# Kernel tuning notes

Hardware: AMD Instinct MI355X
Metric: run time of the kernel (lower is better)

The kernel has to match this reference:

```python
import jax, jax.numpy as jnp
import numpy as np

ITERATIONS = 25  # skeleton_iterations
EPS = 1e-6


def _dilate(x):
    # 3x3 max-pool, stride 1, SAME padding (pads with -inf, matching torch max_pool2d)
    return jax.lax.reduce_window(x, -jnp.inf, jax.lax.max,
                                 (1, 1, 3, 3), (1, 1, 1, 1), 'SAME')


def _erode(x):
    return -_dilate(-x)


def _soft_skeleton(img):
    # img: (B,1,H,W) probability map
    img = jnp.clip(img, 0.0, 1.0)
    skel = jax.nn.relu(img - _dilate(_erode(img)))

    def body(_, carry):
        im, sk = carry
        im = _erode(im)
        delta = jax.nn.relu(im - _dilate(_erode(im)))
        sk = sk + jax.nn.relu(delta - sk * delta)
        return (im, sk)

    _, skel = jax.lax.fori_loop(0, ITERATIONS - 1, body, (img, skel))
    return skel


def setup_inputs() -> dict:
    key = jax.random.key(0)
    k1, k2 = jax.random.split(key)
    B, C, H, W = 8, 19, 512, 512
    return {
        'student_logits': jax.random.normal(k1, (B, C, H, W), dtype=jnp.float32),
        'sam3_pseudo_mask': jax.random.uniform(k2, (B, H, W), dtype=jnp.float32),
        'class_index': 1,
    }


def reference(student_logits, sam3_pseudo_mask, class_index):
    # student probability for target class: (B,1,H,W)
    student_prob = jax.nn.softmax(student_logits, axis=1)[:, class_index:class_index + 1]
    teacher_prob = jnp.clip(sam3_pseudo_mask[:, None, :, :], 0.0, 1.0)

    student_skel = _soft_skeleton(student_prob)
    teacher_skel = _soft_skeleton(teacher_prob)

    rd = (1, 2, 3)
    tprec = (jnp.sum(student_skel * teacher_prob, axis=rd) + EPS) / (jnp.sum(student_skel, axis=rd) + EPS)
    tsens = (jnp.sum(teacher_skel * student_prob, axis=rd) + EPS) / (jnp.sum(teacher_skel, axis=rd) + EPS)
    cldice = (2.0 * tprec * tsens + EPS) / (tprec + tsens + EPS)
    return jnp.mean(1.0 - cldice)
```

## Files before the change

kernel.cpp:

```cpp
#include <hip/hip_runtime.h>

#define B 8
#define C 19
#define H 512
#define W 512
#define P (H*W)
#define NPL 16
#define BIGF 1e30f
#define NT 512
#define HR 14
#define SR 92
#define SC 96
#define E  13

__device__ __forceinline__ float min3f(float a, float b, float c) { return fminf(fminf(a, b), c); }
__device__ __forceinline__ float max3f(float a, float b, float c) { return fmaxf(fmaxf(a, b), c); }

__global__ __launch_bounds__(256) void prep_kernel(
    const float* __restrict__ logits, const float* __restrict__ mask,
    const int* __restrict__ cls, float* __restrict__ prob)
{
    int tid = blockIdx.x * 256 + threadIdx.x;
    const int tot = B * (P / 4);
    if (tid >= tot) return;
    int b  = tid / (P / 4);
    int i4 = tid % (P / 4);
    int ci = *cls;

    const float4* lg = reinterpret_cast<const float4*>(logits) + (size_t)b * C * (P / 4) + i4;
    float4 v[C];
    float4 vc = make_float4(0.f, 0.f, 0.f, 0.f);
    #pragma unroll
    for (int c = 0; c < C; ++c) {
        float4 t = lg[(size_t)c * (P / 4)];
        v[c] = t;
        if (c == ci) vc = t;
    }
    float4 mx = v[0];
    #pragma unroll
    for (int c = 1; c < C; ++c) {
        mx.x = fmaxf(mx.x, v[c].x); mx.y = fmaxf(mx.y, v[c].y);
        mx.z = fmaxf(mx.z, v[c].z); mx.w = fmaxf(mx.w, v[c].w);
    }
    float4 s = make_float4(0.f, 0.f, 0.f, 0.f);
    #pragma unroll
    for (int c = 0; c < C; ++c) {
        s.x += expf(v[c].x - mx.x); s.y += expf(v[c].y - mx.y);
        s.z += expf(v[c].z - mx.z); s.w += expf(v[c].w - mx.w);
    }
    float4 p;
    p.x = expf(vc.x - mx.x) / s.x;
    p.y = expf(vc.y - mx.y) / s.y;
    p.z = expf(vc.z - mx.z) / s.z;
    p.w = expf(vc.w - mx.w) / s.w;

    float4* pr = reinterpret_cast<float4*>(prob);
    pr[(size_t)b * (P / 4) + i4] = p;

    float4 tm = reinterpret_cast<const float4*>(mask)[(size_t)b * (P / 4) + i4];
    tm.x = fminf(fmaxf(tm.x, 0.f), 1.f);
    tm.y = fminf(fmaxf(tm.y, 0.f), 1.f);
    tm.z = fminf(fmaxf(tm.z, 0.f), 1.f);
    tm.w = fminf(fmaxf(tm.w, 0.f), 1.f);
    pr[(size_t)(8 + b) * (P / 4) + i4] = tm;
}

__device__ __forceinline__ void erode_pass(const float* __restrict__ src,
                                           float* __restrict__ dst, int p, int tid)
{
    const int r0 = p;
    const int n  = (SR - 2 * p) * 24;
    const int lane = tid & 63;
    for (int idx = tid; idx < n; idx += NT) {
        int r = r0 + idx / 24, g = idx % 24, c = 4 * g;
        const float* s1 = src + r * SC + c;
        float4 a  = *reinterpret_cast<const float4*>(s1 - SC);
        float4 b  = *reinterpret_cast<const float4*>(s1);
        float4 cc = *reinterpret_cast<const float4*>(s1 + SC);
        float4 vm;
        vm.x = min3f(a.x, b.x, cc.x);
        vm.y = min3f(a.y, b.y, cc.y);
        vm.z = min3f(a.z, b.z, cc.z);
        vm.w = min3f(a.w, b.w, cc.w);
        float vL = __shfl_up(vm.w, 1);
        float vR = __shfl_down(vm.x, 1);
        if (g == 0  || lane == 0)  vL = min3f(s1[-SC - 1], s1[-1], s1[SC - 1]);
        if (g == 23 || lane == 63) vR = min3f(s1[-SC + 4], s1[4], s1[SC + 4]);
        float4 o;
        o.x = min3f(vL,   vm.x, vm.y);
        o.y = min3f(vm.x, vm.y, vm.z);
        o.z = min3f(vm.y, vm.z, vm.w);
        o.w = min3f(vm.z, vm.w, vR);
        *reinterpret_cast<float4*>(dst + r * SC + c) = o;
    }
}

__device__ __forceinline__ float4 dilate4(const float* __restrict__ e,
                                          int lr, int lc, int gy, int gxb,
                                          bool fbL, bool fbR)
{
    const float* p0 = e + (lr - 1) * SC + lc;
    const float* p1 = e + lr * SC + lc;
    const float* p2 = e + (lr + 1) * SC + lc;
    float4 a = *reinterpret_cast<const float4*>(p0);
    float4 b = *reinterpret_cast<const float4*>(p1);
    float4 c = *reinterpret_cast<const float4*>(p2);
    const bool t = (gy > 0), u = (gy < H - 1);
    float4 vm;
    vm.x = fmaxf(b.x, fmaxf(t ? a.x : -BIGF, u ? c.x : -BIGF));
    vm.y = fmaxf(b.y, fmaxf(t ? a.y : -BIGF, u ? c.y : -BIGF));
    vm.z = fmaxf(b.z, fmaxf(t ? a.z : -BIGF, u ? c.z : -BIGF));
    vm.w = fmaxf(b.w, fmaxf(t ? a.w : -BIGF, u ? c.w : -BIGF));
    float vL = __shfl_up(vm.w, 1);
    float vR = __shfl_down(vm.x, 1);
    if (fbL) vL = max3f(t ? p0[-1] : -BIGF, p1[-1], u ? p2[-1] : -BIGF);
    if (fbR) vR = max3f(t ? p0[4]  : -BIGF, p1[4],  u ? p2[4]  : -BIGF);
    if (gxb == 0)     vL = -BIGF;
    if (gxb == W - 4) vR = -BIGF;
    float4 d;
    d.x = max3f(vL,   vm.x, vm.y);
    d.y = max3f(vm.x, vm.y, vm.z);
    d.z = max3f(vm.y, vm.z, vm.w);
    d.w = max3f(vm.z, vm.w, vR);
    return d;
}

template<int MODE>
__global__ __launch_bounds__(NT, 4) void skel_kernel(
    const float* __restrict__ in, float* __restrict__ im_out,
    float* __restrict__ gsk, const float* __restrict__ prob,
    double* __restrict__ sums)
{
    __shared__ __align__(16) float lds[2 * SR * SC + 32];
    float* const bx = lds + 16;
    float* const by = bx + SR * SC;
    const int pl  = blockIdx.z;
    const int ty0 = blockIdx.y * 64, tx0 = blockIdx.x * 64;
    const int tid = threadIdx.x;
    const float* ip = in + (size_t)pl * P;
    const size_t gbase = (size_t)pl * P;

    const int jA  = tid & 15;
    const int pyA = tid >> 4, pyB = pyA + 32;
    const int lcA = 16 + 4 * jA;
    const int lrA = pyA + HR, lrB = pyB + HR;
    const int gyA = ty0 + pyA, gyB = ty0 + pyB;
    const int gxb = tx0 + 4 * jA;
    const bool fbL = (jA == 0)  || ((tid & 63) == 0);
    const bool fbR = (jA == 15) || ((tid & 63) == 63);

    const bool xin = (tx0 >= 16) && (tx0 <= W - 80);
    for (int idx = tid; idx < SR * 24; idx += NT) {
        int r = idx / 24, g = idx % 24;
        int gy = ty0 - HR + r; gy = min(max(gy, 0), H - 1);
        int gx0 = tx0 - 16 + 4 * g;
        float4 v;
        if (xin) {
            v = *reinterpret_cast<const float4*>(ip + (size_t)gy * W + gx0);
        } else {
            const float* rp = ip + (size_t)gy * W;
            v.x = rp[min(max(gx0,     0), W - 1)];
            v.y = rp[min(max(gx0 + 1, 0), W - 1)];
            v.z = rp[min(max(gx0 + 2, 0), W - 1)];
            v.w = rp[min(max(gx0 + 3, 0), W - 1)];
        }
        *reinterpret_cast<float4*>(&bx[r * SC + 4 * g]) = v;
    }

    float4 sk0, sk1;
    if (MODE == 0) {
        sk0 = make_float4(0.f, 0.f, 0.f, 0.f);
        sk1 = sk0;
    } else {
        sk0 = *reinterpret_cast<const float4*>(gsk + gbase + (size_t)gyA * W + gxb);
        sk1 = *reinterpret_cast<const float4*>(gsk + gbase + (size_t)gyB * W + gxb);
    }
    __syncthreads();

    erode_pass(bx, by, 1, tid);
    float4 curA = *reinterpret_cast<const float4*>(bx + lrA * SC + lcA);
    float4 curB = *reinterpret_cast<const float4*>(bx + lrB * SC + lcA);
    __syncthreads();

    for (int p = 2; p <= E; ++p) {
        const float* src = (p & 1) ? bx : by;
        float*       dst = (p & 1) ? by : bx;
        if (MODE == 0 || p > 2) {
            float4 dA = dilate4(src, lrA, lcA, gyA, gxb, fbL, fbR);
            float4 dB = dilate4(src, lrB, lcA, gyB, gxb, fbL, fbR);
            float4 del;
            del.x = fmaxf(curA.x - dA.x, 0.f); del.y = fmaxf(curA.y - dA.y, 0.f);
            del.z = fmaxf(curA.z - dA.z, 0.f); del.w = fmaxf(curA.w - dA.w, 0.f);
            sk0.x += fmaxf(del.x - sk0.x * del.x, 0.f);
            sk0.y += fmaxf(del.y - sk0.y * del.y, 0.f);
            sk0.z += fmaxf(del.z - sk0.z * del.z, 0.f);
            sk0.w += fmaxf(del.w - sk0.w * del.w, 0.f);
            del.x = fmaxf(curB.x - dB.x, 0.f); del.y = fmaxf(curB.y - dB.y, 0.f);
            del.z = fmaxf(curB.z - dB.z, 0.f); del.w = fmaxf(curB.w - dB.w, 0.f);
            sk1.x += fmaxf(del.x - sk1.x * del.x, 0.f);
            sk1.y += fmaxf(del.y - sk1.y * del.y, 0.f);
            sk1.z += fmaxf(del.z - sk1.z * del.z, 0.f);
            sk1.w += fmaxf(del.w - sk1.w * del.w, 0.f);
        }
        float4 nxtA = *reinterpret_cast<const float4*>(src + lrA * SC + lcA);
        float4 nxtB = *reinterpret_cast<const float4*>(src + lrB * SC + lcA);
        erode_pass(src, dst, p, tid);
        __syncthreads();
        curA = nxtA; curB = nxtB;
    }

    {
        float4 dA = dilate4(by, lrA, lcA, gyA, gxb, fbL, fbR);
        float4 dB = dilate4(by, lrB, lcA, gyB, gxb, fbL, fbR);
        float4 del;
        del.x = fmaxf(curA.x - dA.x, 0.f); del.y = fmaxf(curA.y - dA.y, 0.f);
        del.z = fmaxf(curA.z - dA.z, 0.f); del.w = fmaxf(curA.w - dA.w, 0.f);
        sk0.x += fmaxf(del.x - sk0.x * del.x, 0.f);
        sk0.y += fmaxf(del.y - sk0.y * del.y, 0.f);
        sk0.z += fmaxf(del.z - sk0.z * del.z, 0.f);
        sk0.w += fmaxf(del.w - sk0.w * del.w, 0.f);
        del.x = fmaxf(curB.x - dB.x, 0.f); del.y = fmaxf(curB.y - dB.y, 0.f);
        del.z = fmaxf(curB.z - dB.z, 0.f); del.w = fmaxf(curB.w - dB.w, 0.f);
        sk1.x += fmaxf(del.x - sk1.x * del.x, 0.f);
        sk1.y += fmaxf(del.y - sk1.y * del.y, 0.f);
        sk1.z += fmaxf(del.z - sk1.z * del.z, 0.f);
        sk1.w += fmaxf(del.w - sk1.w * del.w, 0.f);
    }

    if (MODE == 0) {
        *reinterpret_cast<float4*>(im_out + gbase + (size_t)gyA * W + gxb) = curA;
        *reinterpret_cast<float4*>(im_out + gbase + (size_t)gyB * W + gxb) = curB;
        *reinterpret_cast<float4*>(gsk + gbase + (size_t)gyA * W + gxb) = sk0;
        *reinterpret_cast<float4*>(gsk + gbase + (size_t)gyB * W + gxb) = sk1;
    } else {
        const float* op = prob + (size_t)(pl ^ 8) * P;
        float4 tA = *reinterpret_cast<const float4*>(op + (size_t)gyA * W + gxb);
        float4 tB = *reinterpret_cast<const float4*>(op + (size_t)gyB * W + gxb);
        float a0 = sk0.x * tA.x + sk0.y * tA.y + sk0.z * tA.z + sk0.w * tA.w
                 + sk1.x * tB.x + sk1.y * tB.y + sk1.z * tB.z + sk1.w * tB.w;
        float a1 = sk0.x + sk0.y + sk0.z + sk0.w + sk1.x + sk1.y + sk1.z + sk1.w;
        #pragma unroll
        for (int off = 32; off > 0; off >>= 1) {
            a0 += __shfl_down(a0, off);
            a1 += __shfl_down(a1, off);
        }
        __syncthreads();
        float* scratch = lds;
        int wv = tid >> 6, ln = tid & 63;
        if (ln == 0) { scratch[wv * 2] = a0; scratch[wv * 2 + 1] = a1; }
        __syncthreads();
        if (tid == 0) {
            double s0 = 0.0, s1 = 0.0;
            for (int w = 0; w < NT / 64; ++w) {
                s0 += (double)scratch[w * 2];
                s1 += (double)scratch[w * 2 + 1];
            }
            int b = pl & 7, base = (pl < 8) ? 0 : 2;
            atomicAdd(&sums[b * 4 + base + 0], s0);
            atomicAdd(&sums[b * 4 + base + 1], s1);
        }
    }
}

__global__ void zero_sums_kernel(double* __restrict__ sums)
{
    if (threadIdx.x < 32) sums[threadIdx.x] = 0.0;
}

__global__ void final_kernel(const double* __restrict__ sums, float* __restrict__ out)
{
    if (threadIdx.x == 0) {
        double acc = 0.0;
        for (int b = 0; b < 8; ++b) {
            double tprec = (sums[b * 4 + 0] + 1e-6) / (sums[b * 4 + 1] + 1e-6);
            double tsens = (sums[b * 4 + 2] + 1e-6) / (sums[b * 4 + 3] + 1e-6);
            double cl    = (2.0 * tprec * tsens + 1e-6) / (tprec + tsens + 1e-6);
            acc += 1.0 - cl;
        }
        out[0] = (float)(acc / 8.0);
    }
}

extern "C" void kernel_launch(void* const* d_in, const int* in_sizes, int n_in,
                              void* d_out, int out_size, void* d_ws, size_t ws_size,
                              hipStream_t stream)
{
    const float* logits = (const float*)d_in[0];
    const float* mask   = (const float*)d_in[1];
    const int*   cls    = (const int*)d_in[2];
    float* out = (float*)d_out;

    float*  ws   = (float*)d_ws;
    float*  prob = ws;
    float*  imA  = ws + (size_t)16 * P;
    float*  gsk  = ws + (size_t)32 * P;
    double* sums = (double*)(ws + (size_t)48 * P);

    dim3 sg(8, 8, NPL);
    zero_sums_kernel<<<1, 64, 0, stream>>>(sums);
    prep_kernel<<<(B * (P / 4) + 255) / 256, 256, 0, stream>>>(logits, mask, cls, prob);
    skel_kernel<0><<<sg, NT, 0, stream>>>(prob, imA, gsk, prob, sums);
    skel_kernel<2><<<sg, NT, 0, stream>>>(imA, nullptr, gsk, prob, sums);
    final_kernel<<<1, 64, 0, stream>>>(sums, out);
}
```

Measured before the change: 384.0 us.

## Fuse dilate with erode per thread-owned pixels and split halo erode work

Inside the skeleton loop, each thread now computes the erode of its two owned 4-pixel groups and, from the same three LDS row loads, the dilate used for the skeleton update. This removes the separate dilate pass's LDS re-reads and the extra center load. Remaining halo columns and rows are eroded by a separate mapping: the extra column groups plus a shrinking set of top and bottom halo rows. Zeroing of the sums buffer moves into the prep kernel, dropping one launch. The new work split changes load balance across threads and adds index logic.

```diff
diff --git a/kernel.cpp b/kernel.cpp
--- a/kernel.cpp
+++ b/kernel.cpp
@@ -15,11 +15,14 @@
 
 __device__ __forceinline__ float min3f(float a, float b, float c) { return fminf(fminf(a, b), c); }
 __device__ __forceinline__ float max3f(float a, float b, float c) { return fmaxf(fmaxf(a, b), c); }
+__device__ __forceinline__ float4 ld4(const float* p) { return *reinterpret_cast<const float4*>(p); }
 
 __global__ __launch_bounds__(256) void prep_kernel(
     const float* __restrict__ logits, const float* __restrict__ mask,
-    const int* __restrict__ cls, float* __restrict__ prob)
-{
+    const int* __restrict__ cls, float* __restrict__ prob,
+    double* __restrict__ sums)
+{
+    if (blockIdx.x == 0 && threadIdx.x < 32) sums[threadIdx.x] = 0.0;
     int tid = blockIdx.x * 256 + threadIdx.x;
     const int tot = B * (P / 4);
     if (tid >= tot) return;
@@ -65,64 +68,110 @@
     pr[(size_t)(8 + b) * (P / 4) + i4] = tm;
 }
 
-__device__ __forceinline__ void erode_pass(const float* __restrict__ src,
-                                           float* __restrict__ dst, int p, int tid)
-{
-    const int r0 = p;
-    const int n  = (SR - 2 * p) * 24;
-    const int lane = tid & 63;
-    for (int idx = tid; idx < n; idx += NT) {
-        int r = r0 + idx / 24, g = idx % 24, c = 4 * g;
-        const float* s1 = src + r * SC + c;
-        float4 a  = *reinterpret_cast<const float4*>(s1 - SC);
-        float4 b  = *reinterpret_cast<const float4*>(s1);
-        float4 cc = *reinterpret_cast<const float4*>(s1 + SC);
-        float4 vm;
-        vm.x = min3f(a.x, b.x, cc.x);
-        vm.y = min3f(a.y, b.y, cc.y);
-        vm.z = min3f(a.z, b.z, cc.z);
-        vm.w = min3f(a.w, b.w, cc.w);
-        float vL = __shfl_up(vm.w, 1);
-        float vR = __shfl_down(vm.x, 1);
-        if (g == 0  || lane == 0)  vL = min3f(s1[-SC - 1], s1[-1], s1[SC - 1]);
-        if (g == 23 || lane == 63) vR = min3f(s1[-SC + 4], s1[4], s1[SC + 4]);
-        float4 o;
-        o.x = min3f(vL,   vm.x, vm.y);
-        o.y = min3f(vm.x, vm.y, vm.z);
-        o.z = min3f(vm.y, vm.z, vm.w);
-        o.w = min3f(vm.z, vm.w, vR);
-        *reinterpret_cast<float4*>(dst + r * SC + c) = o;
-    }
-}
-
-__device__ __forceinline__ float4 dilate4(const float* __restrict__ e,
-                                          int lr, int lc, int gy, int gxb,
-                                          bool fbL, bool fbR)
-{
-    const float* p0 = e + (lr - 1) * SC + lc;
-    const float* p1 = e + lr * SC + lc;
-    const float* p2 = e + (lr + 1) * SC + lc;
-    float4 a = *reinterpret_cast<const float4*>(p0);
-    float4 b = *reinterpret_cast<const float4*>(p1);
-    float4 c = *reinterpret_cast<const float4*>(p2);
-    const bool t = (gy > 0), u = (gy < H - 1);
+__device__ __forceinline__ float4 erode_grp(const float* __restrict__ src,
+                                            int r, int c, bool fL, bool fR)
+{
+    const float* s1 = src + r * SC + c;
+    float4 a = ld4(s1 - SC), b = ld4(s1), cc = ld4(s1 + SC);
     float4 vm;
-    vm.x = fmaxf(b.x, fmaxf(t ? a.x : -BIGF, u ? c.x : -BIGF));
-    vm.y = fmaxf(b.y, fmaxf(t ? a.y : -BIGF, u ? c.y : -BIGF));
-    vm.z = fmaxf(b.z, fmaxf(t ? a.z : -BIGF, u ? c.z : -BIGF));
-    vm.w = fmaxf(b.w, fmaxf(t ? a.w : -BIGF, u ? c.w : -BIGF));
+    vm.x = min3f(a.x, b.x, cc.x);
+    vm.y = min3f(a.y, b.y, cc.y);
+    vm.z = min3f(a.z, b.z, cc.z);
+    vm.w = min3f(a.w, b.w, cc.w);
     float vL = __shfl_up(vm.w, 1);
     float vR = __shfl_down(vm.x, 1);
-    if (fbL) vL = max3f(t ? p0[-1] : -BIGF, p1[-1], u ? p2[-1] : -BIGF);
-    if (fbR) vR = max3f(t ? p0[4]  : -BIGF, p1[4],  u ? p2[4]  : -BIGF);
-    if (gxb == 0)     vL = -BIGF;
-    if (gxb == W - 4) vR = -BIGF;
+    if (fL) vL = min3f(s1[-SC - 1], s1[-1], s1[SC - 1]);
+    if (fR) vR = min3f(s1[-SC + 4], s1[4], s1[SC + 4]);
+    float4 o;
+    o.x = min3f(vL,   vm.x, vm.y);
+    o.y = min3f(vm.x, vm.y, vm.z);
+    o.z = min3f(vm.y, vm.z, vm.w);
+    o.w = min3f(vm.z, vm.w, vR);
+    return o;
+}
+
+template<bool DODIL>
+__device__ __forceinline__ float4 fused_grp(const float* __restrict__ src,
+    int lr, int c, int gy, int gxb, bool fL, bool fR,
+    float4* __restrict__ bcap, float4* __restrict__ dil)
+{
+    const float* s1 = src + lr * SC + c;
+    float4 a = ld4(s1 - SC), b = ld4(s1), cc = ld4(s1 + SC);
+    *bcap = b;
+    float eL0 = 0.f, eL1 = 0.f, eL2 = 0.f, eR0 = 0.f, eR1 = 0.f, eR2 = 0.f;
+    if (fL) { eL0 = s1[-SC - 1]; eL1 = s1[-1]; eL2 = s1[SC - 1]; }
+    if (fR) { eR0 = s1[-SC + 4]; eR1 = s1[4];  eR2 = s1[SC + 4]; }
+    float4 vm;
+    vm.x = min3f(a.x, b.x, cc.x);
+    vm.y = min3f(a.y, b.y, cc.y);
+    vm.z = min3f(a.z, b.z, cc.z);
+    vm.w = min3f(a.w, b.w, cc.w);
+    float vL = __shfl_up(vm.w, 1);
+    float vR = __shfl_down(vm.x, 1);
+    if (fL) vL = min3f(eL0, eL1, eL2);
+    if (fR) vR = min3f(eR0, eR1, eR2);
+    float4 o;
+    o.x = min3f(vL,   vm.x, vm.y);
+    o.y = min3f(vm.x, vm.y, vm.z);
+    o.z = min3f(vm.y, vm.z, vm.w);
+    o.w = min3f(vm.z, vm.w, vR);
+    if (DODIL) {
+        const bool t = (gy > 0), u = (gy < H - 1);
+        float4 xm;
+        xm.x = fmaxf(b.x, fmaxf(t ? a.x : -BIGF, u ? cc.x : -BIGF));
+        xm.y = fmaxf(b.y, fmaxf(t ? a.y : -BIGF, u ? cc.y : -BIGF));
+        xm.z = fmaxf(b.z, fmaxf(t ? a.z : -BIGF, u ? cc.z : -BIGF));
+        xm.w = fmaxf(b.w, fmaxf(t ? a.w : -BIGF, u ? cc.w : -BIGF));
+        float xL = __shfl_up(xm.w, 1);
+        float xR = __shfl_down(xm.x, 1);
+        if (fL) xL = max3f(t ? eL0 : -BIGF, eL1, u ? eL2 : -BIGF);
+        if (fR) xR = max3f(t ? eR0 : -BIGF, eR1, u ? eR2 : -BIGF);
+        if (gxb == 0)     xL = -BIGF;
+        if (gxb == W - 4) xR = -BIGF;
+        dil->x = max3f(xL,   xm.x, xm.y);
+        dil->y = max3f(xm.x, xm.y, xm.z);
+        dil->z = max3f(xm.y, xm.z, xm.w);
+        dil->w = max3f(xm.z, xm.w, xR);
+    }
+    return o;
+}
+
+__device__ __forceinline__ float4 dil_grp(const float* __restrict__ e,
+    int lr, int c, int gy, int gxb, bool fL, bool fR)
+{
+    const float* s1 = e + lr * SC + c;
+    float4 a = ld4(s1 - SC), b = ld4(s1), cc = ld4(s1 + SC);
+    const bool t = (gy > 0), u = (gy < H - 1);
+    float4 xm;
+    xm.x = fmaxf(b.x, fmaxf(t ? a.x : -BIGF, u ? cc.x : -BIGF));
+    xm.y = fmaxf(b.y, fmaxf(t ? a.y : -BIGF, u ? cc.y : -BIGF));
+    xm.z = fmaxf(b.z, fmaxf(t ? a.z : -BIGF, u ? cc.z : -BIGF));
+    xm.w = fmaxf(b.w, fmaxf(t ? a.w : -BIGF, u ? cc.w : -BIGF));
+    float xL = __shfl_up(xm.w, 1);
+    float xR = __shfl_down(xm.x, 1);
+    if (fL) xL = max3f(t ? s1[-SC - 1] : -BIGF, s1[-1], u ? s1[SC - 1] : -BIGF);
+    if (fR) xR = max3f(t ? s1[-SC + 4] : -BIGF, s1[4],  u ? s1[SC + 4] : -BIGF);
+    if (gxb == 0)     xL = -BIGF;
+    if (gxb == W - 4) xR = -BIGF;
     float4 d;
-    d.x = max3f(vL,   vm.x, vm.y);
-    d.y = max3f(vm.x, vm.y, vm.z);
-    d.z = max3f(vm.y, vm.z, vm.w);
-    d.w = max3f(vm.z, vm.w, vR);
+    d.x = max3f(xL,   xm.x, xm.y);
+    d.y = max3f(xm.x, xm.y, xm.z);
+    d.z = max3f(xm.y, xm.z, xm.w);
+    d.w = max3f(xm.z, xm.w, xR);
     return d;
+}
+
+__device__ __forceinline__ void skupd(float4& sk, const float4& cur, const float4& d)
+{
+    float4 del;
+    del.x = fmaxf(cur.x - d.x, 0.f);
+    del.y = fmaxf(cur.y - d.y, 0.f);
+    del.z = fmaxf(cur.z - d.z, 0.f);
+    del.w = fmaxf(cur.w - d.w, 0.f);
+    sk.x += fmaxf(del.x - sk.x * del.x, 0.f);
+    sk.y += fmaxf(del.y - sk.y * del.y, 0.f);
+    sk.z += fmaxf(del.z - sk.z * del.z, 0.f);
+    sk.w += fmaxf(del.w - sk.w * del.w, 0.f);
 }
 
 template<int MODE>
@@ -136,18 +185,24 @@
     float* const by = bx + SR * SC;
     const int pl  = blockIdx.z;
     const int ty0 = blockIdx.y * 64, tx0 = blockIdx.x * 64;
-    const int tid = threadIdx.x;
+    const int tid = threadIdx.x, lane = tid & 63;
     const float* ip = in + (size_t)pl * P;
     const size_t gbase = (size_t)pl * P;
 
-    const int jA  = tid & 15;
-    const int pyA = tid >> 4, pyB = pyA + 32;
-    const int lcA = 16 + 4 * jA;
-    const int lrA = pyA + HR, lrB = pyB + HR;
-    const int gyA = ty0 + pyA, gyB = ty0 + pyB;
-    const int gxb = tx0 + 4 * jA;
-    const bool fbL = (jA == 0)  || ((tid & 63) == 0);
-    const bool fbR = (jA == 15) || ((tid & 63) == 63);
+    const int j   = tid & 15;
+    const int py  = tid >> 4;
+    const int cA  = 16 + 4 * j;
+    const int lrA = 14 + py, lrB = 46 + py;
+    const int gyA = ty0 + py, gyB = gyA + 32;
+    const int gxb = tx0 + 4 * j;
+    const bool fL = (j == 0), fR = (j == 15);
+
+    const int e8 = tid & 7;
+    const int rX = 14 + (tid >> 3);
+    const int gX = (e8 < 4) ? e8 : 16 + e8;
+    const int cX = 4 * gX;
+    const bool xfL = (e8 == 0) || (e8 == 4);
+    const bool xfR = (e8 == 3) || (e8 == 7);
 
     const bool xin = (tx0 >= 16) && (tx0 <= W - 80);
     for (int idx = tid; idx < SR * 24; idx += NT) {
@@ -156,7 +211,7 @@
         int gx0 = tx0 - 16 + 4 * g;
         float4 v;
         if (xin) {
-            v = *reinterpret_cast<const float4*>(ip + (size_t)gy * W + gx0);
+            v = ld4(ip + (size_t)gy * W + gx0);
         } else {
             const float* rp = ip + (size_t)gy * W;
             v.x = rp[min(max(gx0,     0), W - 1)];
@@ -172,59 +227,60 @@
         sk0 = make_float4(0.f, 0.f, 0.f, 0.f);
         sk1 = sk0;
     } else {
-        sk0 = *reinterpret_cast<const float4*>(gsk + gbase + (size_t)gyA * W + gxb);
-        sk1 = *reinterpret_cast<const float4*>(gsk + gbase + (size_t)gyB * W + gxb);
+        sk0 = ld4(gsk + gbase + (size_t)gyA * W + gxb);
+        sk1 = ld4(gsk + gbase + (size_t)gyB * W + gxb);
     }
     __syncthreads();
 
-    erode_pass(bx, by, 1, tid);
-    float4 curA = *reinterpret_cast<const float4*>(bx + lrA * SC + lcA);
-    float4 curB = *reinterpret_cast<const float4*>(bx + lrB * SC + lcA);
+    float4 curA, curB, dump;
+    {
+        float4 oA = fused_grp<false>(bx, lrA, cA, gyA, gxb, fL, fR, &curA, &dump);
+        *reinterpret_cast<float4*>(by + lrA * SC + cA) = oA;
+        float4 oB = fused_grp<false>(bx, lrB, cA, gyB, gxb, fL, fR, &curB, &dump);
+        *reinterpret_cast<float4*>(by + lrB * SC + cA) = oB;
+        float4 oX = erode_grp(bx, rX, cX, xfL, xfR);
+        *reinterpret_cast<float4*>(by + rX * SC + cX) = oX;
+        const int nb = HR - 1;
+        for (int idx = tid; idx < 2 * nb * 24; idx += NT) {
+            int rb = idx / 24, g = idx % 24;
+            int r = (rb < nb) ? 1 + rb : 78 + (rb - nb);
+            bool hfL = (g == 0) || (lane == 0), hfR = (g == 23) || (lane == 63);
+            float4 o = erode_grp(bx, r, 4 * g, hfL, hfR);
+            *reinterpret_cast<float4*>(by + r * SC + 4 * g) = o;
+        }
+    }
     __syncthreads();
 
     for (int p = 2; p <= E; ++p) {
         const float* src = (p & 1) ? bx : by;
         float*       dst = (p & 1) ? by : bx;
-        if (MODE == 0 || p > 2) {
-            float4 dA = dilate4(src, lrA, lcA, gyA, gxb, fbL, fbR);
-            float4 dB = dilate4(src, lrB, lcA, gyB, gxb, fbL, fbR);
-            float4 del;
-            del.x = fmaxf(curA.x - dA.x, 0.f); del.y = fmaxf(curA.y - dA.y, 0.f);
-            del.z = fmaxf(curA.z - dA.z, 0.f); del.w = fmaxf(curA.w - dA.w, 0.f);
-            sk0.x += fmaxf(del.x - sk0.x * del.x, 0.f);
-            sk0.y += fmaxf(del.y - sk0.y * del.y, 0.f);
-            sk0.z += fmaxf(del.z - sk0.z * del.z, 0.f);
-            sk0.w += fmaxf(del.w - sk0.w * del.w, 0.f);
-            del.x = fmaxf(curB.x - dB.x, 0.f); del.y = fmaxf(curB.y - dB.y, 0.f);
-            del.z = fmaxf(curB.z - dB.z, 0.f); del.w = fmaxf(curB.w - dB.w, 0.f);
-            sk1.x += fmaxf(del.x - sk1.x * del.x, 0.f);
-            sk1.y += fmaxf(del.y - sk1.y * del.y, 0.f);
-            sk1.z += fmaxf(del.z - sk1.z * del.z, 0.f);
-            sk1.w += fmaxf(del.w - sk1.w * del.w, 0.f);
-        }
-        float4 nxtA = *reinterpret_cast<const float4*>(src + lrA * SC + lcA);
-        float4 nxtB = *reinterpret_cast<const float4*>(src + lrB * SC + lcA);
-        erode_pass(src, dst, p, tid);
+        float4 nA, nB, dA, dB;
+        float4 oA = fused_grp<true>(src, lrA, cA, gyA, gxb, fL, fR, &nA, &dA);
+        *reinterpret_cast<float4*>(dst + lrA * SC + cA) = oA;
+        if (MODE == 0 || p > 2) skupd(sk0, curA, dA);
+        curA = nA;
+        float4 oB = fused_grp<true>(src, lrB, cA, gyB, gxb, fL, fR, &nB, &dB);
+        *reinterpret_cast<float4*>(dst + lrB * SC + cA) = oB;
+        if (MODE == 0 || p > 2) skupd(sk1, curB, dB);
+        curB = nB;
+        float4 oX = erode_grp(src, rX, cX, xfL, xfR);
+        *reinterpret_cast<float4*>(dst + rX * SC + cX) = oX;
+        const int nb = HR - p;
+        for (int idx = tid; idx < 2 * nb * 24; idx += NT) {
+            int rb = idx / 24, g = idx % 24;
+            int r = (rb < nb) ? p + rb : 78 + (rb - nb);
+            bool hfL = (g == 0) || (lane == 0), hfR = (g == 23) || (lane == 63);
+            float4 o = erode_grp(src, r, 4 * g, hfL, hfR);
+            *reinterpret_cast<float4*>(dst + r * SC + 4 * g) = o;
+        }
         __syncthreads();
-        curA = nxtA; curB = nxtB;
     }
 
     {
-        float4 dA = dilate4(by, lrA, lcA, gyA, gxb, fbL, fbR);
-        float4 dB = dilate4(by, lrB, lcA, gyB, gxb, fbL, fbR);
-        float4 del;
-        del.x = fmaxf(curA.x - dA.x, 0.f); del.y = fmaxf(curA.y - dA.y, 0.f);
-        del.z = fmaxf(curA.z - dA.z, 0.f); del.w = fmaxf(curA.w - dA.w, 0.f);
-        sk0.x += fmaxf(del.x - sk0.x * del.x, 0.f);
-        sk0.y += fmaxf(del.y - sk0.y * del.y, 0.f);
-        sk0.z += fmaxf(del.z - sk0.z * del.z, 0.f);
-        sk0.w += fmaxf(del.w - sk0.w * del.w, 0.f);
-        del.x = fmaxf(curB.x - dB.x, 0.f); del.y = fmaxf(curB.y - dB.y, 0.f);
-        del.z = fmaxf(curB.z - dB.z, 0.f); del.w = fmaxf(curB.w - dB.w, 0.f);
-        sk1.x += fmaxf(del.x - sk1.x * del.x, 0.f);
-        sk1.y += fmaxf(del.y - sk1.y * del.y, 0.f);
-        sk1.z += fmaxf(del.z - sk1.z * del.z, 0.f);
-        sk1.w += fmaxf(del.w - sk1.w * del.w, 0.f);
+        float4 dA = dil_grp(by, lrA, cA, gyA, gxb, fL, fR);
+        float4 dB = dil_grp(by, lrB, cA, gyB, gxb, fL, fR);
+        skupd(sk0, curA, dA);
+        skupd(sk1, curB, dB);
     }
 
     if (MODE == 0) {
@@ -234,8 +290,8 @@
         *reinterpret_cast<float4*>(gsk + gbase + (size_t)gyB * W + gxb) = sk1;
     } else {
         const float* op = prob + (size_t)(pl ^ 8) * P;
-        float4 tA = *reinterpret_cast<const float4*>(op + (size_t)gyA * W + gxb);
-        float4 tB = *reinterpret_cast<const float4*>(op + (size_t)gyB * W + gxb);
+        float4 tA = ld4(op + (size_t)gyA * W + gxb);
+        float4 tB = ld4(op + (size_t)gyB * W + gxb);
         float a0 = sk0.x * tA.x + sk0.y * tA.y + sk0.z * tA.z + sk0.w * tA.w
                  + sk1.x * tB.x + sk1.y * tB.y + sk1.z * tB.z + sk1.w * tB.w;
         float a1 = sk0.x + sk0.y + sk0.z + sk0.w + sk1.x + sk1.y + sk1.z + sk1.w;
@@ -262,11 +318,6 @@
     }
 }
 
-__global__ void zero_sums_kernel(double* __restrict__ sums)
-{
-    if (threadIdx.x < 32) sums[threadIdx.x] = 0.0;
-}
-
 __global__ void final_kernel(const double* __restrict__ sums, float* __restrict__ out)
 {
     if (threadIdx.x == 0) {
@@ -297,8 +348,7 @@
     double* sums = (double*)(ws + (size_t)48 * P);
 
     dim3 sg(8, 8, NPL);
-    zero_sums_kernel<<<1, 64, 0, stream>>>(sums);
-    prep_kernel<<<(B * (P / 4) + 255) / 256, 256, 0, stream>>>(logits, mask, cls, prob);
+    prep_kernel<<<(B * (P / 4) + 255) / 256, 256, 0, stream>>>(logits, mask, cls, prob, sums);
     skel_kernel<0><<<sg, NT, 0, stream>>>(prob, imA, gsk, prob, sums);
     skel_kernel<2><<<sg, NT, 0, stream>>>(imA, nullptr, gsk, prob, sums);
     final_kernel<<<1, 64, 0, stream>>>(sums, out);
```

New measurement: 364.0 us. -5.2%, faster.
